# Kernel tuning notes

Measured on AMD Instinct MI355X. Metric: run time of the kernel, lower is better.

Reference implementation:

```python
import jax, jax.numpy as jnp
import numpy as np

HEADS = 4

def _pair_msg(H, w2, B, xsrc):
    # H:[E,mid] radial-MLP hidden; w2:[mid,co,ci,nf]; B:[E,m_out,m_in,nf] CG/SH basis; xsrc:[E,ci,m_in]
    tmp = jnp.einsum('epqf,eiq->eipf', B, xsrc)          # basis-weighted input  [E,ci,m_out,nf]
    R = jnp.einsum('eh,hoif->eoif', H, w2)               # per-edge radial weights [E,co,ci,nf]
    return jnp.einsum('eoif,eipf->eop', R, tmp)          # edge message [E,co,m_out]

def _conv_edges(ef, w1, w2_nf1, w2_11, b00, b01, b10, b11, x0s, x1s):
    # pair index p = 2*d_in + d_out; pairs (0,0),(0,1),(1,0) have nf=1, pair (1,1) has nf=3
    H = jax.nn.relu(jnp.einsum('ef,pfh->peh', ef, w1))
    m0 = _pair_msg(H[0], w2_nf1[0][..., None], b00, x0s) + _pair_msg(H[2], w2_nf1[2][..., None], b10, x1s)
    m1 = _pair_msg(H[1], w2_nf1[1][..., None], b01, x0s) + _pair_msg(H[3], w2_11, b11, x1s)
    return m0, m1

def _seg_softmax(z, dst, n):
    m = jax.ops.segment_max(z, dst, num_segments=n)
    m = jnp.where(jnp.isfinite(m), m, 0.0)
    e = jnp.exp(z - m[dst])
    s = jax.ops.segment_sum(e, dst, num_segments=n)
    return e / (s[dst] + 1e-9)

def _norm_se3(x, g, b, eps=1e-3):
    n = jnp.sqrt((x * x).sum(-1) + 1e-12)                # per-channel irrep norm [N,C]
    mu = n.mean(-1, keepdims=True)
    var = ((n - mu) ** 2).mean(-1, keepdims=True)
    ln = (n - mu) / jnp.sqrt(var + 1e-5) * g + b
    return x * (jax.nn.relu(ln) / (n + eps))[..., None]

def _forward(x0, x1, edge_feat, b00, b01, b10, b11, kv_w1, kv_w2_nf1, kv_w2_11,
             wq, wproj, norm_gamma, norm_beta, fc_w1, fc_w2_nf1, fc_w2_11, fc_wself,
             edge_src, edge_dst):
    N = x0.shape[0]
    E = edge_src.shape[0]
    L = kv_w1.shape[0]
    ckv = wq.shape[-1]
    scale = 1.0 / np.sqrt((ckv // HEADS) * 4)            # key feats per head over degrees 0,1 (1+3 comps)
    hs = lambda t: t.reshape(t.shape[0], HEADS, ckv // HEADS, t.shape[-1])
    for l in range(L):
        # AttentionBlockSE3: ConvSE3 -> per-edge key/value; LinearSE3 -> query; seg-softmax attention
        kv0, kv1 = _conv_edges(edge_feat, kv_w1[l], kv_w2_nf1[l], kv_w2_11[l],
                               b00, b01, b10, b11, x0[edge_src], x1[edge_src])
        k0, v0 = kv0[:, :ckv], kv0[:, ckv:]
        k1, v1 = kv1[:, :ckv], kv1[:, ckv:]
        q0 = jnp.einsum('ncm,cd->ndm', x0, wq[l, 0])
        q1 = jnp.einsum('ncm,cd->ndm', x1, wq[l, 1])
        z = (hs(q0)[edge_dst] * hs(k0)).sum((2, 3)) + (hs(q1)[edge_dst] * hs(k1)).sum((2, 3))
        alpha = _seg_softmax(z * scale, edge_dst, N)     # [E,heads]
        a0 = (alpha[:, :, None, None] * hs(v0)).reshape(E, ckv, 1)
        a1 = (alpha[:, :, None, None] * hs(v1)).reshape(E, ckv, 3)
        o0 = jax.ops.segment_sum(a0, edge_dst, num_segments=N)
        o1 = jax.ops.segment_sum(a1, edge_dst, num_segments=N)
        # project concat(attn_out, skip) per degree, then NormSE3
        x0 = jnp.einsum('ncm,cd->ndm', jnp.concatenate([o0, x0], 1), wproj[l, 0])
        x1 = jnp.einsum('ncm,cd->ndm', jnp.concatenate([o1, x1], 1), wproj[l, 1])
        x0 = _norm_se3(x0, norm_gamma[l, 0], norm_beta[l, 0])
        x1 = _norm_se3(x1, norm_gamma[l, 1], norm_beta[l, 1])
    # final ConvSE3 with self-interaction, scatter-aggregated over dst nodes
    m0, m1 = _conv_edges(edge_feat, fc_w1, fc_w2_nf1, fc_w2_11,
                         b00, b01, b10, b11, x0[edge_src], x1[edge_src])
    y0 = jax.ops.segment_sum(m0, edge_dst, num_segments=N) + jnp.einsum('ncm,cd->ndm', x0, fc_wself[0])
    y1 = jax.ops.segment_sum(m1, edge_dst, num_segments=N) + jnp.einsum('ncm,cd->ndm', x1, fc_wself[1])
    return jnp.concatenate([y0.reshape(N, -1), y1.reshape(N, -1)], axis=1)

def setup_inputs() -> dict:
    key = jax.random.key(0)
    ks = jax.random.split(key, 20)
    N, E, C, L = 8192, 131072, 16, 2
    Fe, mid, KV, ckv, Co = 16, 16, 16, 8, 8
    f = lambda k, s, sc=1.0: jax.random.normal(k, s, dtype=jnp.float32) * sc
    return {
        'x0': f(ks[0], (N, C, 1)),
        'x1': f(ks[1], (N, C, 3)),
        'edge_feat': f(ks[2], (E, Fe)),
        'b00': f(ks[3], (E, 1, 1, 1)),
        'b01': f(ks[4], (E, 3, 1, 1)),
        'b10': f(ks[5], (E, 1, 3, 1)),
        'b11': f(ks[6], (E, 3, 3, 3)),
        'kv_w1': f(ks[7], (L, 4, Fe, mid), 0.1),
        'kv_w2_nf1': f(ks[8], (L, 3, mid, KV, C), 0.1),
        'kv_w2_11': f(ks[9], (L, mid, KV, C, 3), 0.1),
        'wq': f(ks[10], (L, 2, C, ckv), 0.1),
        'wproj': f(ks[11], (L, 2, ckv + C, C), 0.1),
        'norm_gamma': jnp.ones((L, 2, C), dtype=jnp.float32),
        'norm_beta': jnp.zeros((L, 2, C), dtype=jnp.float32),
        'fc_w1': f(ks[12], (4, Fe, mid), 0.1),
        'fc_w2_nf1': f(ks[13], (3, mid, Co, C), 0.1),
        'fc_w2_11': f(ks[14], (mid, Co, C, 3), 0.1),
        'fc_wself': f(ks[15], (2, C, Co), 0.1),
        'edge_src': jax.random.randint(ks[16], (E,), 0, N, dtype=jnp.int32),
        'edge_dst': jax.random.randint(ks[17], (E,), 0, N, dtype=jnp.int32),
    }

def reference(x0, x1, edge_feat, b00, b01, b10, b11, kv_w1, kv_w2_nf1, kv_w2_11,
              wq, wproj, norm_gamma, norm_beta, fc_w1, fc_w2_nf1, fc_w2_11, fc_wself,
              edge_src, edge_dst):
    return _forward(x0, x1, edge_feat, b00, b01, b10, b11, kv_w1, kv_w2_nf1, kv_w2_11,
                    wq, wproj, norm_gamma, norm_beta, fc_w1, fc_w2_nf1, fc_w2_11, fc_wself,
                    edge_src, edge_dst)
```

## Files before the change

kernel.cpp:

```cpp
#include <hip/hip_runtime.h>
#include <hip/hip_fp16.h>
#include <math.h>


typedef _Float16 half8 __attribute__((ext_vector_type(8)));
typedef float f32x4 __attribute__((ext_vector_type(4)));

union AF {
    half8 h8;
    __half2 h2[4];
};
union U32h2 {
    unsigned u;
    __half2 h;
};

__global__ void k_hist(const int* __restrict__ dst, int* __restrict__ counts, int E) {
    int e = blockIdx.x * 256 + threadIdx.x;
    if (e < E) atomicAdd(&counts[dst[e]], 1);
}

__global__ __launch_bounds__(1024) void k_scan(const int* __restrict__ counts,
                                               int* __restrict__ rowptr,
                                               int* __restrict__ cursor,
                                               int N, int CH) {
    __shared__ int part[1024];
    int t = threadIdx.x;
    int s = 0;
    for (int i = 0; i < CH; ++i) {
        int idx = t * CH + i;
        if (idx < N) s += counts[idx];
    }
    part[t] = s;
    __syncthreads();
    for (int off = 1; off < 1024; off <<= 1) {
        int v = (t >= off) ? part[t - off] : 0;
        __syncthreads();
        part[t] += v;
        __syncthreads();
    }
    int run = (t == 0) ? 0 : part[t - 1];
    for (int i = 0; i < CH; ++i) {
        int idx = t * CH + i;
        if (idx < N) {
            rowptr[idx] = run;
            cursor[idx] = run;
            run += counts[idx];
        }
    }
    if (t == 0) rowptr[N] = part[1023];
}

__global__ void k_scatter(const int* __restrict__ dst, int* __restrict__ cursor,
                          int* __restrict__ pose, int E) {
    int e = blockIdx.x * 256 + threadIdx.x;
    if (e < E) {
        int pos = atomicAdd(&cursor[dst[e]], 1);
        pose[e] = pos;
    }
}

__global__ void k_init(const float* __restrict__ x0, const float* __restrict__ x1,
                       const float* __restrict__ ef,
                       const float* __restrict__ kvw1, const float* __restrict__ fcw1,
                       const float* __restrict__ kvw2n, const float* __restrict__ kvw211,
                       const float* __restrict__ fcw2n, const float* __restrict__ fcw211,
                       const float* __restrict__ wq,
                       float* __restrict__ xs0, float* __restrict__ xs1,
                       unsigned short* __restrict__ efh,
                       unsigned short* __restrict__ Wfrag,
                       float* __restrict__ q0, float* __restrict__ q1,
                       int N, int E) {
    int i = blockIdx.x * 256 + threadIdx.x;
    if (i < 156 * 64 * 8) {
        int t = i;
        int j = t & 7;
        int lane = (t >> 3) & 63;
        int row = t >> 9;
        int quad = lane >> 4, m = lane & 15;
        int c = row / 52, r = row % 52;
        int KVO = (c < 2) ? 16 : 8;
        const float* w1src = (c < 2) ? (kvw1 + c * 1024) : fcw1;
        const float* w2n = (c < 2) ? (kvw2n + c * 12288) : fcw2n;
        const float* w211 = (c < 2) ? (kvw211 + c * 12288) : fcw211;
        float v = 0.f;
        if (r < 4) {
            if (quad < 2) v = w1src[r * 256 + (quad * 8 + j) * 16 + m];
        } else if (r < 28) {
            int fam = (r - 4) >> 3, kk = (r - 4) & 7;
            int h = quad * 4 + ((j >> 1) & 3), ii = 2 * kk + (j & 1);
            if (m < KVO) v = w2n[((fam * 16 + h) * KVO + m) * 16 + ii];
        } else {
            int kk2 = r - 28;
            int h = quad * 4 + ((j >> 1) & 3);
            int ifx = 2 * kk2 + (j & 1);
            int ii = ifx / 3, f = ifx % 3;
            if (m < KVO) v = w211[((h * KVO + m) * 16 + ii) * 3 + f];
        }
        Wfrag[t] = __half_as_ushort(__float2half(v));
        return;
    }
    i -= 156 * 64 * 8;
    if (i < N * 16) { xs0[i] = x0[i]; return; }
    i -= N * 16;
    if (i < N * 48) { xs1[i] = x1[i]; return; }
    i -= N * 48;
    if (i < E * 16) { efh[i] = __half_as_ushort(__float2half(ef[i])); return; }
    i -= E * 16;
    if (i < N * 32) {
        int n = i >> 5, comp = i & 31;
        if (comp < 8) {
            float a = 0.f;
#pragma unroll
            for (int c = 0; c < 16; ++c) a += x0[n * 16 + c] * wq[c * 8 + comp];
            q0[n * 8 + comp] = a;
        } else {
            int idx = comp - 8, dd = idx / 3, mm = idx % 3;
            float a = 0.f;
#pragma unroll
            for (int c = 0; c < 16; ++c) a += x1[n * 48 + c * 3 + mm] * wq[128 + c * 8 + dd];
            q1[n * 24 + dd * 3 + mm] = a;
        }
    }
}

template <int KVO, bool DO_Z>
__global__ __launch_bounds__(256) void k_conv(
    int E,
    const int* __restrict__ src, const int* __restrict__ dst,
    const int* __restrict__ pose,
    const float* __restrict__ xs0, const float* __restrict__ xs1,
    const float* __restrict__ b00, const float* __restrict__ b01,
    const float* __restrict__ b10, const float* __restrict__ b11,
    const unsigned short* __restrict__ efh,
    const unsigned short* __restrict__ Wfrag,
    int wbase,
    const float* __restrict__ q0, const float* __restrict__ q1,
    float* __restrict__ vrow, float* __restrict__ zb)
{
    __shared__ __align__(16) unsigned xBL[4][16 * 74];
    __shared__ float b11L[4][16 * 29];
    int tid = threadIdx.x;
    int wave = tid >> 6, lane = tid & 63;
    int tile = blockIdx.x * 4 + wave;
    if (tile * 16 >= E) return;
    int m = lane & 15, quad = lane >> 4;
    int e0 = tile * 16;
    int me = e0 + m;
    int s = src[me];
    unsigned* xw = xBL[wave];
    const half8* W8 = (const half8*)Wfrag;

    {
        const float* gb = b11 + (size_t)e0 * 27;
        float* lb = b11L[wave];
#pragma unroll
        for (int it = 0; it < 7; ++it) {
            int d = it * 64 + lane;
            if (d < 432) {
                int ee = d / 27, kk = d - ee * 27;
                lb[ee * 29 + kk] = gb[d];
            }
        }
    }
    __syncthreads();

    {
        float x1c[12];
        const float4* xp = (const float4*)(xs1 + (size_t)s * 48 + quad * 12);
#pragma unroll
        for (int cc = 0; cc < 3; ++cc) {
            float4 v = xp[cc];
            x1c[cc * 4 + 0] = v.x; x1c[cc * 4 + 1] = v.y;
            x1c[cc * 4 + 2] = v.z; x1c[cc * 4 + 3] = v.w;
        }
        const float* lb = &b11L[wave][m * 29];
        float b11r[27];
#pragma unroll
        for (int k = 0; k < 27; ++k) b11r[k] = lb[k];
#pragma unroll
        for (int p = 0; p < 3; ++p) {
            float vals[12];
#pragma unroll
            for (int i2 = 0; i2 < 4; ++i2) {
#pragma unroll
                for (int f = 0; f < 3; ++f) {
                    float a = 0.f;
#pragma unroll
                    for (int q = 0; q < 3; ++q) a += x1c[i2 * 3 + q] * b11r[p * 9 + q * 3 + f];
                    vals[i2 * 3 + f] = a;
                }
            }
            unsigned uu[6];
#pragma unroll
            for (int u = 0; u < 6; ++u) {
                U32h2 w;
                w.h = __float22half2_rn(make_float2(vals[2 * u], vals[2 * u + 1]));
                uu[u] = w.u;
            }
            int boff = m * 74 + p * 24 + quad * 6;
            *(uint2*)&xw[boff + 0] = make_uint2(uu[0], uu[1]);
            *(uint2*)&xw[boff + 2] = make_uint2(uu[2], uu[3]);
            *(uint2*)&xw[boff + 4] = make_uint2(uu[4], uu[5]);
        }
    }
    __syncthreads();

    __half2 x0p[8], t10p[8];
    {
        const float4* p = (const float4*)(xs0 + (size_t)s * 16);
#pragma unroll
        for (int k = 0; k < 4; ++k) {
            float4 v = p[k];
            x0p[2 * k + 0] = __float22half2_rn(make_float2(v.x, v.y));
            x0p[2 * k + 1] = __float22half2_rn(make_float2(v.z, v.w));
        }
        float bq0 = b10[(size_t)me * 3 + 0], bq1 = b10[(size_t)me * 3 + 1],
              bq2 = b10[(size_t)me * 3 + 2];
        const float4* xp = (const float4*)(xs1 + (size_t)s * 48);
        float tf[16];
#pragma unroll
        for (int g = 0; g < 4; ++g) {
            float4 a = xp[g * 3 + 0], b = xp[g * 3 + 1], cc = xp[g * 3 + 2];
            float xf[12] = {a.x, a.y, a.z, a.w, b.x, b.y, b.z, b.w, cc.x, cc.y, cc.z, cc.w};
#pragma unroll
            for (int i2 = 0; i2 < 4; ++i2)
                tf[g * 4 + i2] = bq0 * xf[i2 * 3] + bq1 * xf[i2 * 3 + 1] + bq2 * xf[i2 * 3 + 2];
        }
#pragma unroll
        for (int k = 0; k < 8; ++k)
            t10p[k] = __float22half2_rn(make_float2(tf[2 * k], tf[2 * k + 1]));
    }

    __half2 Hd[4][4];
    {
        half8 efr = {0, 0, 0, 0, 0, 0, 0, 0};
        if (quad < 2) efr = *(const half8*)(efh + (size_t)me * 16 + quad * 8);
        f32x4 z4 = {0.f, 0.f, 0.f, 0.f};
#pragma unroll
        for (int pp = 0; pp < 4; ++pp) {
            half8 w1f = W8[(size_t)(wbase + pp) * 64 + lane];
            f32x4 hacc = __builtin_amdgcn_mfma_f32_16x16x32_f16(w1f, efr, z4, 0, 0, 0);
#pragma unroll
            for (int r = 0; r < 4; ++r)
                Hd[pp][r] = __float2half2_rn(__float2half(fmaxf(hacc[r], 0.f)));
        }
    }

    f32x4 acc0 = {0.f, 0.f, 0.f, 0.f}, acc1 = acc0, acc2 = acc0;
    f32x4 accP0 = acc0, accP1 = acc0, accP2 = acc0;

#pragma unroll
    for (int kk = 0; kk < 8; ++kk) {
        __half2 xp_ = x0p[kk], tp_ = t10p[kk];
        AF a0, a1, a2;
#pragma unroll
        for (int t = 0; t < 4; ++t) {
            a0.h2[t] = __hmul2(Hd[0][t], xp_);
            a1.h2[t] = __hmul2(Hd[1][t], xp_);
            a2.h2[t] = __hmul2(Hd[2][t], tp_);
        }
        half8 w0 = W8[(size_t)(wbase + 4 + kk) * 64 + lane];
        half8 w1f = W8[(size_t)(wbase + 12 + kk) * 64 + lane];
        half8 w2f = W8[(size_t)(wbase + 20 + kk) * 64 + lane];
        acc0 = __builtin_amdgcn_mfma_f32_16x16x32_f16(w0, a0.h8, acc0, 0, 0, 0);
        acc1 = __builtin_amdgcn_mfma_f32_16x16x32_f16(w1f, a1.h8, acc1, 0, 0, 0);
        acc2 = __builtin_amdgcn_mfma_f32_16x16x32_f16(w2f, a2.h8, acc2, 0, 0, 0);
    }

#pragma unroll
    for (int kko = 0; kko < 12; ++kko) {
        uint2 xu0 = *(const uint2*)&xw[m * 74 + 0 * 24 + 2 * kko];
        uint2 xu1 = *(const uint2*)&xw[m * 74 + 1 * 24 + 2 * kko];
        uint2 xu2 = *(const uint2*)&xw[m * 74 + 2 * 24 + 2 * kko];
        unsigned pv0[2] = {xu0.x, xu0.y};
        unsigned pv1[2] = {xu1.x, xu1.y};
        unsigned pv2[2] = {xu2.x, xu2.y};
#pragma unroll
        for (int t = 0; t < 2; ++t) {
            U32h2 u0, u1, u2;
            u0.u = pv0[t]; u1.u = pv1[t]; u2.u = pv2[t];
            AF a0, a1, a2;
#pragma unroll
            for (int r = 0; r < 4; ++r) {
                a0.h2[r] = __hmul2(Hd[3][r], u0.h);
                a1.h2[r] = __hmul2(Hd[3][r], u1.h);
                a2.h2[r] = __hmul2(Hd[3][r], u2.h);
            }
            half8 wf = W8[(size_t)(wbase + 28 + 2 * kko + t) * 64 + lane];
            accP0 = __builtin_amdgcn_mfma_f32_16x16x32_f16(wf, a0.h8, accP0, 0, 0, 0);
            accP1 = __builtin_amdgcn_mfma_f32_16x16x32_f16(wf, a1.h8, accP1, 0, 0, 0);
            accP2 = __builtin_amdgcn_mfma_f32_16x16x32_f16(wf, a2.h8, accP2, 0, 0, 0);
        }
    }

    float b00r = b00[me];
    float b01r0 = b01[(size_t)me * 3 + 0], b01r1 = b01[(size_t)me * 3 + 1],
          b01r2 = b01[(size_t)me * 3 + 2];
    float o0v[4], o1v[4][3];
#pragma unroll
    for (int r = 0; r < 4; ++r) {
        o0v[r] = b00r * acc0[r] + acc2[r];
        o1v[r][0] = b01r0 * acc1[r] + accP0[r];
        o1v[r][1] = b01r1 * acc1[r] + accP1[r];
        o1v[r][2] = b01r2 * acc1[r] + accP2[r];
    }
    int pos = pose[me];
    bool doStore = DO_Z ? (quad >= 2) : (quad < 2);
    if (doStore) {
        int qa = DO_Z ? (quad - 2) : quad;
        float* vp = vrow + (size_t)pos * 32;
        *(float4*)&vp[qa * 4] = make_float4(o0v[0], o0v[1], o0v[2], o0v[3]);
        float* p1 = vp + 8 + qa * 12;
        *(float4*)&p1[0] = make_float4(o1v[0][0], o1v[0][1], o1v[0][2], o1v[1][0]);
        *(float4*)&p1[4] = make_float4(o1v[1][1], o1v[1][2], o1v[2][0], o1v[2][1]);
        *(float4*)&p1[8] = make_float4(o1v[2][2], o1v[3][0], o1v[3][1], o1v[3][2]);
    }
    if (DO_Z && quad < 2) {
        int n = dst[me];
        float4 q0v = *(const float4*)&q0[(size_t)n * 8 + quad * 4];
        const float4* q1p = (const float4*)&q1[(size_t)n * 24 + quad * 12];
        float4 qa4 = q1p[0], qb4 = q1p[1], qc4 = q1p[2];
        float q1f[12] = {qa4.x, qa4.y, qa4.z, qa4.w, qb4.x, qb4.y, qb4.z, qb4.w,
                         qc4.x, qc4.y, qc4.z, qc4.w};
        float q0f[4] = {q0v.x, q0v.y, q0v.z, q0v.w};
        float zh0 = 0.f, zh1 = 0.f;
#pragma unroll
        for (int r = 0; r < 4; ++r) {
            float tt = q0f[r] * o0v[r] + q1f[r * 3 + 0] * o1v[r][0] +
                       q1f[r * 3 + 1] * o1v[r][1] + q1f[r * 3 + 2] * o1v[r][2];
            if (r < 2) zh0 += tt;
            else zh1 += tt;
        }
        const float scale = 0.35355339059327373f;
        *(float2*)&zb[(size_t)pos * 4 + quad * 2] = make_float2(zh0 * scale, zh1 * scale);
    }
}

__global__ __launch_bounds__(256) void k_attn(
    int N,
    const int* __restrict__ rowptr,
    const float* __restrict__ zb, const float* __restrict__ vrow,
    const float* __restrict__ wproj,
    const float* __restrict__ gamma, const float* __restrict__ beta,
    float* __restrict__ xs0, float* __restrict__ xs1,
    const float* __restrict__ wq_next,
    float* __restrict__ q0, float* __restrict__ q1) {
    __shared__ float wpL[768];
    __shared__ float gL[32], btL[32];
    __shared__ float inb[16][100];
    __shared__ float aw[16][16][4];
    int tid = threadIdx.x;
    for (int i = tid; i < 768; i += 256) wpL[i] = wproj[i];
    if (tid < 32) { gL[tid] = gamma[tid]; btL[tid] = beta[tid]; }
    int wave = tid >> 6, lane = tid & 63;
    int sub = lane >> 4, l16 = lane & 15;
    int nodeIdx = wave * 4 + sub;
    int n = blockIdx.x * 16 + nodeIdx;
    if (n >= N) n = N - 1;
    int base = rowptr[n], deg = rowptr[n + 1] - base;
    const float4* zb4 = (const float4*)zb;

    float mx0 = -INFINITY, mx1 = -INFINITY, mx2 = -INFINITY, mx3 = -INFINITY;
    for (int j = l16; j < deg; j += 16) {
        float4 zv = zb4[base + j];
        mx0 = fmaxf(mx0, zv.x); mx1 = fmaxf(mx1, zv.y);
        mx2 = fmaxf(mx2, zv.z); mx3 = fmaxf(mx3, zv.w);
    }
#pragma unroll
    for (int off = 1; off < 16; off <<= 1) {
        mx0 = fmaxf(mx0, __shfl_xor(mx0, off));
        mx1 = fmaxf(mx1, __shfl_xor(mx1, off));
        mx2 = fmaxf(mx2, __shfl_xor(mx2, off));
        mx3 = fmaxf(mx3, __shfl_xor(mx3, off));
    }
    if (!isfinite(mx0)) mx0 = 0.f;
    if (!isfinite(mx1)) mx1 = 0.f;
    if (!isfinite(mx2)) mx2 = 0.f;
    if (!isfinite(mx3)) mx3 = 0.f;

    int c0 = 2 * l16, c1 = c0 + 1;
    int hA = ((c0 < 8) ? c0 : (c0 - 8) / 3) >> 1;
    int hB = ((c1 < 8) ? c1 : (c1 - 8) / 3) >> 1;
    float s0 = 0.f, s1 = 0.f, s2 = 0.f, s3 = 0.f;
    float accA = 0.f, accB = 0.f;
    for (int j0 = 0; j0 < deg; j0 += 16) {
        int j = j0 + l16;
        float4 a4 = make_float4(0.f, 0.f, 0.f, 0.f);
        if (j < deg) {
            float4 zv = zb4[base + j];
            a4.x = __expf(zv.x - mx0);
            a4.y = __expf(zv.y - mx1);
            a4.z = __expf(zv.z - mx2);
            a4.w = __expf(zv.w - mx3);
            s0 += a4.x; s1 += a4.y; s2 += a4.z; s3 += a4.w;
        }
        *(float4*)&aw[nodeIdx][l16][0] = a4;
        __builtin_amdgcn_wave_barrier();
        int cnt = min(16, deg - j0);
        const float* vbase = &vrow[(size_t)(base + j0) * 32 + c0];
        int jj = 0;
        for (; jj + 3 < cnt; jj += 4) {
            float2 v0 = *(const float2*)(vbase + (size_t)jj * 32);
            float2 v1 = *(const float2*)(vbase + (size_t)(jj + 1) * 32);
            float2 v2 = *(const float2*)(vbase + (size_t)(jj + 2) * 32);
            float2 v3 = *(const float2*)(vbase + (size_t)(jj + 3) * 32);
            accA += aw[nodeIdx][jj][hA] * v0.x + aw[nodeIdx][jj + 1][hA] * v1.x +
                    aw[nodeIdx][jj + 2][hA] * v2.x + aw[nodeIdx][jj + 3][hA] * v3.x;
            accB += aw[nodeIdx][jj][hB] * v0.y + aw[nodeIdx][jj + 1][hB] * v1.y +
                    aw[nodeIdx][jj + 2][hB] * v2.y + aw[nodeIdx][jj + 3][hB] * v3.y;
        }
        for (; jj < cnt; ++jj) {
            float2 v = *(const float2*)(vbase + (size_t)jj * 32);
            accA += aw[nodeIdx][jj][hA] * v.x;
            accB += aw[nodeIdx][jj][hB] * v.y;
        }
        __builtin_amdgcn_wave_barrier();
    }
#pragma unroll
    for (int off = 1; off < 16; off <<= 1) {
        s0 += __shfl_xor(s0, off); s1 += __shfl_xor(s1, off);
        s2 += __shfl_xor(s2, off); s3 += __shfl_xor(s3, off);
    }
    float inva[4] = {1.f / (s0 + 1e-9f), 1.f / (s1 + 1e-9f),
                     1.f / (s2 + 1e-9f), 1.f / (s3 + 1e-9f)};
    accA *= inva[hA];
    accB *= inva[hB];

    float* in0 = inb[nodeIdx];
    float* in1 = in0 + 24;
    if (c0 < 8) { in0[c0] = accA; in0[c1] = accB; }
    else        { in1[c0 - 8] = accA; in1[c1 - 8] = accB; }
    in0[8 + l16] = xs0[(size_t)n * 16 + l16];
    {
        const float* xp = xs1 + (size_t)n * 48 + l16 * 3;
        in1[24 + l16 * 3 + 0] = xp[0];
        in1[24 + l16 * 3 + 1] = xp[1];
        in1[24 + l16 * 3 + 2] = xp[2];
    }
    __syncthreads();

    int c = l16;
    float y0 = 0.f;
#pragma unroll
    for (int j = 0; j < 24; ++j) y0 += in0[j] * wpL[j * 16 + c];
    float y1v[3];
#pragma unroll
    for (int mm = 0; mm < 3; ++mm) {
        float y = 0.f;
#pragma unroll
        for (int j = 0; j < 24; ++j) y += in1[j * 3 + mm] * wpL[384 + j * 16 + c];
        y1v[mm] = y;
    }
    float n0 = sqrtf(y0 * y0 + 1e-12f);
    float n1 = sqrtf(y1v[0] * y1v[0] + y1v[1] * y1v[1] + y1v[2] * y1v[2] + 1e-12f);
    float mu0 = n0, mu1 = n1;
#pragma unroll
    for (int off = 1; off < 16; off <<= 1) {
        mu0 += __shfl_xor(mu0, off);
        mu1 += __shfl_xor(mu1, off);
    }
    mu0 *= 0.0625f; mu1 *= 0.0625f;
    float dv0 = n0 - mu0, dv1 = n1 - mu1;
    float var0 = dv0 * dv0, var1 = dv1 * dv1;
#pragma unroll
    for (int off = 1; off < 16; off <<= 1) {
        var0 += __shfl_xor(var0, off);
        var1 += __shfl_xor(var1, off);
    }
    var0 *= 0.0625f; var1 *= 0.0625f;
    float ln0 = dv0 * rsqrtf(var0 + 1e-5f) * gL[c] + btL[c];
    float ln1 = dv1 * rsqrtf(var1 + 1e-5f) * gL[16 + c] + btL[16 + c];
    float fac0 = fmaxf(ln0, 0.f) / (n0 + 1e-3f);
    float fac1 = fmaxf(ln1, 0.f) / (n1 + 1e-3f);
    float x0n = y0 * fac0;
    float x1n[3] = {y1v[0] * fac1, y1v[1] * fac1, y1v[2] * fac1};
    xs0[(size_t)n * 16 + c] = x0n;
    float* xo = xs1 + (size_t)n * 48 + c * 3;
    xo[0] = x1n[0]; xo[1] = x1n[1]; xo[2] = x1n[2];

    if (wq_next) {
        __builtin_amdgcn_wave_barrier();
        in0[8 + c] = x0n;
        in1[24 + c * 3 + 0] = x1n[0];
        in1[24 + c * 3 + 1] = x1n[1];
        in1[24 + c * 3 + 2] = x1n[2];
        __builtin_amdgcn_wave_barrier();
        int compA = 2 * l16, compB = compA + 1;
#pragma unroll
        for (int cb = 0; cb < 2; ++cb) {
            int comp = cb ? compB : compA;
            float a = 0.f;
            if (comp < 8) {
#pragma unroll
                for (int cc = 0; cc < 16; ++cc)
                    a += in0[8 + cc] * wq_next[cc * 8 + comp];
                q0[(size_t)n * 8 + comp] = a;
            } else {
                int idx = comp - 8, dd = idx / 3, mm = idx % 3;
#pragma unroll
                for (int cc = 0; cc < 16; ++cc)
                    a += in1[24 + cc * 3 + mm] * wq_next[128 + cc * 8 + dd];
                q1[(size_t)n * 24 + idx] = a;
            }
        }
    }
}

__global__ __launch_bounds__(256) void k_out(
    int N,
    const int* __restrict__ rowptr, const float* __restrict__ vrow,
    const float* __restrict__ xs0, const float* __restrict__ xs1,
    const float* __restrict__ wself,
    float* __restrict__ out) {
    int tid = threadIdx.x;
    int wave = tid >> 6, lane = tid & 63;
    int sub = lane >> 4, l16 = lane & 15;
    int n = blockIdx.x * 16 + wave * 4 + sub;
    if (n >= N) n = N - 1;
    int base = rowptr[n], deg = rowptr[n + 1] - base;

    int c0 = 2 * l16, c1 = c0 + 1;
    float accA = 0.f, accB = 0.f;
    const float* vbase = &vrow[(size_t)base * 32 + c0];
    int j = 0;
    for (; j + 3 < deg; j += 4) {
        float2 v0 = *(const float2*)(vbase + (size_t)j * 32);
        float2 v1 = *(const float2*)(vbase + (size_t)(j + 1) * 32);
        float2 v2 = *(const float2*)(vbase + (size_t)(j + 2) * 32);
        float2 v3 = *(const float2*)(vbase + (size_t)(j + 3) * 32);
        accA += v0.x + v1.x + v2.x + v3.x;
        accB += v0.y + v1.y + v2.y + v3.y;
    }
    for (; j < deg; ++j) {
        float2 v = *(const float2*)(vbase + (size_t)j * 32);
        accA += v.x;
        accB += v.y;
    }
    if (c0 < 8) {
#pragma unroll
        for (int c = 0; c < 16; ++c) {
            float xv = xs0[(size_t)n * 16 + c];
            accA += xv * wself[c * 8 + c0];
            accB += xv * wself[c * 8 + c1];
        }
    } else {
        int dA = (c0 - 8) / 3, mA = (c0 - 8) % 3;
        int dB = (c1 - 8) / 3, mB = (c1 - 8) % 3;
#pragma unroll
        for (int c = 0; c < 16; ++c) {
            accA += xs1[(size_t)n * 48 + c * 3 + mA] * wself[128 + c * 8 + dA];
            accB += xs1[(size_t)n * 48 + c * 3 + mB] * wself[128 + c * 8 + dB];
        }
    }
    *(float2*)&out[(size_t)n * 32 + c0] = make_float2(accA, accB);
}

extern "C" void kernel_launch(void* const* d_in, const int* in_sizes, int n_in,
                              void* d_out, int out_size, void* d_ws, size_t ws_size,
                              hipStream_t stream) {
    const float* x0 = (const float*)d_in[0];
    const float* x1 = (const float*)d_in[1];
    const float* ef = (const float*)d_in[2];
    const float* b00 = (const float*)d_in[3];
    const float* b01 = (const float*)d_in[4];
    const float* b10 = (const float*)d_in[5];
    const float* b11 = (const float*)d_in[6];
    const float* kvw1 = (const float*)d_in[7];
    const float* kvw2n = (const float*)d_in[8];
    const float* kvw211 = (const float*)d_in[9];
    const float* wq = (const float*)d_in[10];
    const float* wproj = (const float*)d_in[11];
    const float* gam = (const float*)d_in[12];
    const float* bet = (const float*)d_in[13];
    const float* fcw1 = (const float*)d_in[14];
    const float* fcw2n = (const float*)d_in[15];
    const float* fcw211 = (const float*)d_in[16];
    const float* fcself = (const float*)d_in[17];
    const int* esrc = (const int*)d_in[18];
    const int* edst = (const int*)d_in[19];
    int N = in_sizes[0] / 16;
    int E = in_sizes[18];
    float* out = (float*)d_out;

    float* ws = (float*)d_ws;
    size_t off = 0;
    float* xs0 = ws + off; off += (size_t)N * 16;
    float* xs1 = ws + off; off += (size_t)N * 48;
    float* q0b = ws + off; off += (size_t)N * 8;
    float* q1b = ws + off; off += (size_t)N * 24;
    float* vrow = ws + off; off += (size_t)E * 32;
    float* zb = ws + off; off += (size_t)E * 4;
    int* counts = (int*)(ws + off); off += N;
    int* rowptr = (int*)(ws + off); off += N + 1;
    int* cursor = (int*)(ws + off); off += N;
    int* pose = (int*)(ws + off); off += E;
    off = (off + 3) & ~(size_t)3;
    unsigned short* efh = (unsigned short*)(ws + off); off += (size_t)E * 16 / 2;
    unsigned short* Wfrag = (unsigned short*)(ws + off); off += (size_t)156 * 64 * 8 / 2;

    const int tpb = 256;
    int ebl = (E + 255) / 256;
    int cblk = (E / 16 + 3) / 4;
    int nbl16 = (N + 15) / 16;

    int itot = 156 * 512 + N * 16 + N * 48 + E * 16 + N * 32;
    k_init<<<(itot + 255) / 256, tpb, 0, stream>>>(x0, x1, ef, kvw1, fcw1, kvw2n, kvw211,
                                                   fcw2n, fcw211, wq, xs0, xs1, efh,
                                                   Wfrag, q0b, q1b, N, E);
    hipMemsetAsync(counts, 0, (size_t)N * 4, stream);
    k_hist<<<ebl, tpb, 0, stream>>>(edst, counts, E);
    int CH = (N + 1023) / 1024;
    k_scan<<<1, 1024, 0, stream>>>(counts, rowptr, cursor, N, CH);
    k_scatter<<<ebl, tpb, 0, stream>>>(edst, cursor, pose, E);

    k_conv<16, true><<<cblk, tpb, 0, stream>>>(E, esrc, edst, pose, xs0, xs1,
                                               b00, b01, b10, b11, efh, Wfrag, 0,
                                               q0b, q1b, vrow, zb);
    k_attn<<<nbl16, tpb, 0, stream>>>(N, rowptr, zb, vrow, wproj,
                                      gam, bet, xs0, xs1, wq + 256, q0b, q1b);
    k_conv<16, true><<<cblk, tpb, 0, stream>>>(E, esrc, edst, pose, xs0, xs1,
                                               b00, b01, b10, b11, efh, Wfrag, 52,
                                               q0b, q1b, vrow, zb);
    k_attn<<<nbl16, tpb, 0, stream>>>(N, rowptr, zb, vrow, wproj + 768,
                                      gam + 32, bet + 32, xs0, xs1, nullptr, q0b, q1b);
    k_conv<8, false><<<cblk, tpb, 0, stream>>>(E, esrc, edst, pose, xs0, xs1,
                                               b00, b01, b10, b11, efh, Wfrag, 104,
                                               q0b, q1b, vrow, zb);
    k_out<<<nbl16, tpb, 0, stream>>>(N, rowptr, vrow, xs0, xs1, fcself, out);
}
```

Before: 299.0 us.

## Pre-convert b11 basis to padded fp16 and drop x0/x1 staging copies

The init kernel now converts the per-edge b11 basis once into a 28-wide fp16 buffer. Each conv lane loads its 27 coefficients directly with vector loads, which removes the shared-memory staging and the __syncthreads. The x0/x1 copies into the workspace are also removed: the first layer reads the inputs directly, and the attention kernel takes separate residual-read pointers. This trades some fp16 precision on the basis coefficients and extra init work for less traffic in the three conv launches. The second attention call passes xs0/xs1 as both read and write, which relies on per-node access ordering.

```diff
diff --git a/kernel.cpp b/kernel.cpp
--- a/kernel.cpp
+++ b/kernel.cpp
@@ -14,6 +14,13 @@
     unsigned u;
     __half2 h;
 };
+
+static __device__ __forceinline__ float h2f_lo(unsigned u) {
+    U32h2 w; w.u = u; return __low2float(w.h);
+}
+static __device__ __forceinline__ float h2f_hi(unsigned u) {
+    U32h2 w; w.u = u; return __high2float(w.h);
+}
 
 __global__ void k_hist(const int* __restrict__ dst, int* __restrict__ counts, int E) {
     int e = blockIdx.x * 256 + threadIdx.x;
@@ -61,15 +68,15 @@
 }
 
 __global__ void k_init(const float* __restrict__ x0, const float* __restrict__ x1,
-                       const float* __restrict__ ef,
+                       const float* __restrict__ ef, const float* __restrict__ b11,
                        const float* __restrict__ kvw1, const float* __restrict__ fcw1,
                        const float* __restrict__ kvw2n, const float* __restrict__ kvw211,
                        const float* __restrict__ fcw2n, const float* __restrict__ fcw211,
                        const float* __restrict__ wq,
-                       float* __restrict__ xs0, float* __restrict__ xs1,
                        unsigned short* __restrict__ efh,
                        unsigned short* __restrict__ Wfrag,
                        float* __restrict__ q0, float* __restrict__ q1,
+                       unsigned short* __restrict__ b11h,
                        int N, int E) {
     int i = blockIdx.x * 256 + threadIdx.x;
     if (i < 156 * 64 * 8) {
@@ -101,10 +108,6 @@
         return;
     }
     i -= 156 * 64 * 8;
-    if (i < N * 16) { xs0[i] = x0[i]; return; }
-    i -= N * 16;
-    if (i < N * 48) { xs1[i] = x1[i]; return; }
-    i -= N * 48;
     if (i < E * 16) { efh[i] = __half_as_ushort(__float2half(ef[i])); return; }
     i -= E * 16;
     if (i < N * 32) {
@@ -121,6 +124,12 @@
             for (int c = 0; c < 16; ++c) a += x1[n * 48 + c * 3 + mm] * wq[128 + c * 8 + dd];
             q1[n * 24 + dd * 3 + mm] = a;
         }
+        return;
+    }
+    i -= N * 32;
+    if (i < E * 27) {
+        int e = i / 27, k = i - e * 27;
+        b11h[(size_t)e * 28 + k] = __half_as_ushort(__float2half(b11[i]));
     }
 }
 
@@ -131,7 +140,8 @@
     const int* __restrict__ pose,
     const float* __restrict__ xs0, const float* __restrict__ xs1,
     const float* __restrict__ b00, const float* __restrict__ b01,
-    const float* __restrict__ b10, const float* __restrict__ b11,
+    const float* __restrict__ b10,
+    const unsigned short* __restrict__ b11h,
     const unsigned short* __restrict__ efh,
     const unsigned short* __restrict__ Wfrag,
     int wbase,
@@ -139,7 +149,6 @@
     float* __restrict__ vrow, float* __restrict__ zb)
 {
     __shared__ __align__(16) unsigned xBL[4][16 * 74];
-    __shared__ float b11L[4][16 * 29];
     int tid = threadIdx.x;
     int wave = tid >> 6, lane = tid & 63;
     int tile = blockIdx.x * 4 + wave;
@@ -152,20 +161,6 @@
     const half8* W8 = (const half8*)Wfrag;
 
     {
-        const float* gb = b11 + (size_t)e0 * 27;
-        float* lb = b11L[wave];
-#pragma unroll
-        for (int it = 0; it < 7; ++it) {
-            int d = it * 64 + lane;
-            if (d < 432) {
-                int ee = d / 27, kk = d - ee * 27;
-                lb[ee * 29 + kk] = gb[d];
-            }
-        }
-    }
-    __syncthreads();
-
-    {
         float x1c[12];
         const float4* xp = (const float4*)(xs1 + (size_t)s * 48 + quad * 12);
 #pragma unroll
@@ -174,10 +169,22 @@
             x1c[cc * 4 + 0] = v.x; x1c[cc * 4 + 1] = v.y;
             x1c[cc * 4 + 2] = v.z; x1c[cc * 4 + 3] = v.w;
         }
-        const float* lb = &b11L[wave][m * 29];
         float b11r[27];
-#pragma unroll
-        for (int k = 0; k < 27; ++k) b11r[k] = lb[k];
+        {
+            const uint2* bp = (const uint2*)(b11h + (size_t)me * 28);
+#pragma unroll
+            for (int t = 0; t < 6; ++t) {
+                uint2 uu = bp[t];
+                b11r[4 * t + 0] = h2f_lo(uu.x);
+                b11r[4 * t + 1] = h2f_hi(uu.x);
+                b11r[4 * t + 2] = h2f_lo(uu.y);
+                b11r[4 * t + 3] = h2f_hi(uu.y);
+            }
+            uint2 uu = bp[6];
+            b11r[24] = h2f_lo(uu.x);
+            b11r[25] = h2f_hi(uu.x);
+            b11r[26] = h2f_lo(uu.y);
+        }
 #pragma unroll
         for (int p = 0; p < 3; ++p) {
             float vals[12];
@@ -343,6 +350,7 @@
     const float* __restrict__ zb, const float* __restrict__ vrow,
     const float* __restrict__ wproj,
     const float* __restrict__ gamma, const float* __restrict__ beta,
+    const float* __restrict__ xr0, const float* __restrict__ xr1,
     float* __restrict__ xs0, float* __restrict__ xs1,
     const float* __restrict__ wq_next,
     float* __restrict__ q0, float* __restrict__ q1) {
@@ -431,9 +439,9 @@
     float* in1 = in0 + 24;
     if (c0 < 8) { in0[c0] = accA; in0[c1] = accB; }
     else        { in1[c0 - 8] = accA; in1[c1 - 8] = accB; }
-    in0[8 + l16] = xs0[(size_t)n * 16 + l16];
+    in0[8 + l16] = xr0[(size_t)n * 16 + l16];
     {
-        const float* xp = xs1 + (size_t)n * 48 + l16 * 3;
+        const float* xp = xr1 + (size_t)n * 48 + l16 * 3;
         in1[24 + l16 * 3 + 0] = xp[0];
         in1[24 + l16 * 3 + 1] = xp[1];
         in1[24 + l16 * 3 + 2] = xp[2];
@@ -597,6 +605,7 @@
     int* pose = (int*)(ws + off); off += E;
     off = (off + 3) & ~(size_t)3;
     unsigned short* efh = (unsigned short*)(ws + off); off += (size_t)E * 16 / 2;
+    unsigned short* b11h = (unsigned short*)(ws + off); off += (size_t)E * 28 / 2;
     unsigned short* Wfrag = (unsigned short*)(ws + off); off += (size_t)156 * 64 * 8 / 2;
 
     const int tpb = 256;
@@ -604,28 +613,28 @@
     int cblk = (E / 16 + 3) / 4;
     int nbl16 = (N + 15) / 16;
 
-    int itot = 156 * 512 + N * 16 + N * 48 + E * 16 + N * 32;
-    k_init<<<(itot + 255) / 256, tpb, 0, stream>>>(x0, x1, ef, kvw1, fcw1, kvw2n, kvw211,
-                                                   fcw2n, fcw211, wq, xs0, xs1, efh,
-                                                   Wfrag, q0b, q1b, N, E);
+    int itot = 156 * 512 + E * 16 + N * 32 + E * 27;
+    k_init<<<(itot + 255) / 256, tpb, 0, stream>>>(x0, x1, ef, b11, kvw1, fcw1, kvw2n,
+                                                   kvw211, fcw2n, fcw211, wq, efh,
+                                                   Wfrag, q0b, q1b, b11h, N, E);
     hipMemsetAsync(counts, 0, (size_t)N * 4, stream);
     k_hist<<<ebl, tpb, 0, stream>>>(edst, counts, E);
     int CH = (N + 1023) / 1024;
     k_scan<<<1, 1024, 0, stream>>>(counts, rowptr, cursor, N, CH);
     k_scatter<<<ebl, tpb, 0, stream>>>(edst, cursor, pose, E);
 
+    k_conv<16, true><<<cblk, tpb, 0, stream>>>(E, esrc, edst, pose, x0, x1,
+                                               b00, b01, b10, b11h, efh, Wfrag, 0,
+                                               q0b, q1b, vrow, zb);
+    k_attn<<<nbl16, tpb, 0, stream>>>(N, rowptr, zb, vrow, wproj, gam, bet,
+                                      x0, x1, xs0, xs1, wq + 256, q0b, q1b);
     k_conv<16, true><<<cblk, tpb, 0, stream>>>(E, esrc, edst, pose, xs0, xs1,
-                                               b00, b01, b10, b11, efh, Wfrag, 0,
+                                               b00, b01, b10, b11h, efh, Wfrag, 52,
                                                q0b, q1b, vrow, zb);
-    k_attn<<<nbl16, tpb, 0, stream>>>(N, rowptr, zb, vrow, wproj,
-                                      gam, bet, xs0, xs1, wq + 256, q0b, q1b);
-    k_conv<16, true><<<cblk, tpb, 0, stream>>>(E, esrc, edst, pose, xs0, xs1,
-                                               b00, b01, b10, b11, efh, Wfrag, 52,
-                                               q0b, q1b, vrow, zb);
-    k_attn<<<nbl16, tpb, 0, stream>>>(N, rowptr, zb, vrow, wproj + 768,
-                                      gam + 32, bet + 32, xs0, xs1, nullptr, q0b, q1b);
+    k_attn<<<nbl16, tpb, 0, stream>>>(N, rowptr, zb, vrow, wproj + 768, gam + 32,
+                                      bet + 32, xs0, xs1, xs0, xs1, nullptr, q0b, q1b);
     k_conv<8, false><<<cblk, tpb, 0, stream>>>(E, esrc, edst, pose, xs0, xs1,
-                                               b00, b01, b10, b11, efh, Wfrag, 104,
+                                               b00, b01, b10, b11h, efh, Wfrag, 104,
                                                q0b, q1b, vrow, zb);
     k_out<<<nbl16, tpb, 0, stream>>>(N, rowptr, vrow, xs0, xs1, fcself, out);
 }
```

Measured after the change: 291.9 us. 1.02x faster.
